# Optimization experiments

Hardware: AMD Instinct MI355X
Metric: run time of the kernel (lower is better)

The kernel has to match this reference:

```python
import jax, jax.numpy as jnp
import numpy as np

EPS_COS = 1e-8   # torch cosine_similarity eps
EPS_SHARP = 1e-6 # sharpening normalizer eps
SHIFT_RANGE = 3
MEM_WIDTH = 64


def setup_inputs() -> dict:
    key = jax.random.key(0)
    k1, k2, k3, k4, k5 = jax.random.split(key, 5)
    B, H, N, W, D = 64, 4, 16384, MEM_WIDTH, 1024
    P = W + 6  # key(W) + beta + gate + shift(3) + gamma
    return {
        "controller_state": jax.random.normal(k1, (B, D), dtype=jnp.float32),
        "prev_weights": jax.random.uniform(k2, (B, H, N), dtype=jnp.float32),
        "memory": jax.random.normal(k3, (B, N, W), dtype=jnp.float32),
        "W_read": jax.random.normal(k4, (P * H, D), dtype=jnp.float32) * 0.02,
        "b_read": jax.random.normal(k5, (P * H,), dtype=jnp.float32) * 0.02,
    }


def reference(controller_state, prev_weights, memory, W_read, b_read):
    B, H, N = prev_weights.shape
    Wd = MEM_WIDTH
    # read head parameters: [B, H, P]
    params = (controller_state @ W_read.T + b_read).reshape(B, H, -1)
    key = params[..., :Wd]                                   # [B,H,W]
    beta = jax.nn.softplus(params[..., Wd])                  # [B,H]
    gate = jax.nn.sigmoid(params[..., Wd + 1])               # [B,H]
    shift = jax.nn.softmax(params[..., Wd + 2:Wd + 2 + SHIFT_RANGE], axis=-1)  # [B,H,3]
    gamma = 1.0 + jax.nn.softplus(params[..., Wd + 2 + SHIFT_RANGE])           # [B,H]

    # content addressing: cosine similarity of key vs each memory slot
    dots = jnp.einsum('bhw,bnw->bhn', key, memory)           # [B,H,N]
    key_norm = jnp.maximum(jnp.linalg.norm(key, axis=-1), EPS_COS)        # [B,H]
    mem_norm = jnp.maximum(jnp.linalg.norm(memory, axis=-1), EPS_COS)     # [B,N]
    sim = dots / (key_norm[:, :, None] * mem_norm[:, None, :])
    content_w = jax.nn.softmax(sim * beta[:, :, None], axis=-1)           # [B,H,N]

    # interpolate with previous weights
    g = gate[:, :, None]
    gated = g * content_w + (1.0 - g) * prev_weights                     # [B,H,N]

    # circular shift: out[pos] = s0*w[pos-1] + s1*w[pos] + s2*w[pos+1]
    shifted = (shift[..., 0:1] * jnp.roll(gated, 1, axis=-1)
               + shift[..., 1:2] * gated
               + shift[..., 2:3] * jnp.roll(gated, -1, axis=-1))

    # sharpening
    sharp = shifted ** gamma[:, :, None]
    sharp = sharp / (jnp.sum(sharp, axis=-1, keepdims=True) + EPS_SHARP)
    return sharp  # [B,H,N]
```

## Files before the change

kernel.cpp:

```cpp
#include <hip/hip_runtime.h>
#include <math.h>

#define B  64
#define H  4
#define NN 16384
#define WD 64
#define DD 1024
#define PP 70

typedef float fx4 __attribute__((ext_vector_type(4)));

__device__ __forceinline__ float softplus_f(float x) {
    return fmaxf(x, 0.f) + log1pf(expf(-fabsf(x)));
}

__global__ __launch_bounds__(256) void k_params(
    const float* __restrict__ state, const float* __restrict__ Wr,
    const float* __restrict__ br, float* __restrict__ kscaled,
    float* __restrict__ coef)
{
    int bh = blockIdx.x;
    int b  = bh >> 2, h = bh & 3;
    int tid = threadIdx.x, wave = tid >> 6, lane = tid & 63;
    __shared__ float sp[PP];
    __shared__ float sbc[1];

    const float4* st4 = (const float4*)(state + (size_t)b * DD);
    for (int j = wave; j < PP; j += 4) {
        const float4* w4 = (const float4*)(Wr + (size_t)(h * PP + j) * DD);
        float acc = 0.f;
        #pragma unroll
        for (int q = 0; q < 4; ++q) {
            float4 wv = w4[lane + 64 * q];
            float4 sv = st4[lane + 64 * q];
            acc += wv.x * sv.x + wv.y * sv.y + wv.z * sv.z + wv.w * sv.w;
        }
        #pragma unroll
        for (int m = 32; m >= 1; m >>= 1) acc += __shfl_xor(acc, m, 64);
        if (lane == 0) sp[j] = acc + br[h * PP + j];
    }
    __syncthreads();
    if (tid == 0) {
        float ss = 0.f;
        for (int w = 0; w < WD; ++w) ss += sp[w] * sp[w];
        float knorm = fmaxf(sqrtf(ss), 1e-8f);
        float beta  = softplus_f(sp[64]);
        float gate  = 1.f / (1.f + expf(-sp[65]));
        float m3 = fmaxf(sp[66], fmaxf(sp[67], sp[68]));
        float e0 = expf(sp[66] - m3), e1 = expf(sp[67] - m3), e2 = expf(sp[68] - m3);
        float es = e0 + e1 + e2;
        float gamma = 1.f + softplus_f(sp[69]);
        float* c = coef + bh * 8;
        c[0] = gate; c[1] = e0 / es; c[2] = e1 / es; c[3] = e2 / es;
        c[4] = gamma; c[5] = beta;
        sbc[0] = beta / knorm;
    }
    __syncthreads();
    if (tid < WD) kscaled[bh * WD + tid] = sp[tid] * sbc[0];
}

__global__ __launch_bounds__(256) void k_sim(
    const float* __restrict__ mem, const float* __restrict__ kscaled,
    const float* __restrict__ coef, float* __restrict__ ebuf)
{
    int tid = threadIdx.x, wave = tid >> 6, lane = tid & 63;
    int blk = blockIdx.x;
    int b = blk >> 7;
    int nblk = (blk & 127) * 128;
    int r = lane >> 3, c = lane & 7;

    const float* ksb = kscaled + b * 4 * WD + c * 8;
    float4 k0a = *(const float4*)(ksb + 0 * WD);
    float4 k0b = *(const float4*)(ksb + 0 * WD + 4);
    float4 k1a = *(const float4*)(ksb + 1 * WD);
    float4 k1b = *(const float4*)(ksb + 1 * WD + 4);
    float4 k2a = *(const float4*)(ksb + 2 * WD);
    float4 k2b = *(const float4*)(ksb + 2 * WD + 4);
    float4 k3a = *(const float4*)(ksb + 3 * WD);
    float4 k3b = *(const float4*)(ksb + 3 * WD + 4);

    float bet = (c < 4) ? coef[(b * 4 + c) * 8 + 5] : 0.f;

    int nw = nblk + wave * 32;
    fx4 va[4], vb[4];
    #pragma unroll
    for (int it = 0; it < 4; ++it) {
        int n = nw + it * 8 + r;
        const fx4* rp = (const fx4*)(mem + ((size_t)b * NN + n) * WD + c * 8);
        va[it] = __builtin_nontemporal_load(rp);
        vb[it] = __builtin_nontemporal_load(rp + 1);
    }
    #pragma unroll
    for (int it = 0; it < 4; ++it) {
        fx4 v0 = va[it], v1 = vb[it];
        int n = nw + it * 8 + r;
        float d0 = v0.x*k0a.x + v0.y*k0a.y + v0.z*k0a.z + v0.w*k0a.w
                 + v1.x*k0b.x + v1.y*k0b.y + v1.z*k0b.z + v1.w*k0b.w;
        float d1 = v0.x*k1a.x + v0.y*k1a.y + v0.z*k1a.z + v0.w*k1a.w
                 + v1.x*k1b.x + v1.y*k1b.y + v1.z*k1b.z + v1.w*k1b.w;
        float d2 = v0.x*k2a.x + v0.y*k2a.y + v0.z*k2a.z + v0.w*k2a.w
                 + v1.x*k2b.x + v1.y*k2b.y + v1.z*k2b.z + v1.w*k2b.w;
        float d3 = v0.x*k3a.x + v0.y*k3a.y + v0.z*k3a.z + v0.w*k3a.w
                 + v1.x*k3b.x + v1.y*k3b.y + v1.z*k3b.z + v1.w*k3b.w;
        float q  = v0.x*v0.x + v0.y*v0.y + v0.z*v0.z + v0.w*v0.w
                 + v1.x*v1.x + v1.y*v1.y + v1.z*v1.z + v1.w*v1.w;
        #pragma unroll
        for (int m = 1; m < 8; m <<= 1) {
            d0 += __shfl_xor(d0, m, 64);
            d1 += __shfl_xor(d1, m, 64);
            d2 += __shfl_xor(d2, m, 64);
            d3 += __shfl_xor(d3, m, 64);
            q  += __shfl_xor(q,  m, 64);
        }
        if (c < 4) {
            float mn = fmaxf(sqrtf(q), 1e-8f);
            float d  = (c == 0) ? d0 : ((c == 1) ? d1 : ((c == 2) ? d2 : d3));
            ebuf[((size_t)(b * 4 + c)) * NN + n] = __expf(d / mn - bet);
        }
    }
}

__global__ __launch_bounds__(1024) void k_head(
    const float* __restrict__ ebuf, const float* __restrict__ prev,
    const float* __restrict__ coef, float* __restrict__ out)
{
    __shared__ float lds[NN];
    int bh = blockIdx.x;
    int tid = threadIdx.x, wave = tid >> 6, lane = tid & 63;
    const float* erow = ebuf + (size_t)bh * NN;
    const float* prow = prev + (size_t)bh * NN;
    float* orow = out + (size_t)bh * NN;
    const float* c = coef + bh * 8;
    float gate = c[0], sh0 = c[1], sh1 = c[2], sh2 = c[3], gamma = c[4];

    float ev[16], pw[16];
    float ls = 0.f;
    #pragma unroll
    for (int k = 0; k < 16; ++k) {
        int n = tid + k * 1024;
        ev[k] = erow[n];
        pw[k] = prow[n];
        ls += ev[k];
    }
    #pragma unroll
    for (int d = 32; d >= 1; d >>= 1) ls += __shfl_xor(ls, d, 64);
    if (lane == 0) lds[wave] = ls;
    __syncthreads();
    if (tid == 0) {
        float x = 0.f;
        for (int i = 0; i < 16; ++i) x += lds[i];
        lds[16] = x;
    }
    __syncthreads();
    float S = lds[16];
    __syncthreads();
    float ginvS = gate / S;
    float omg   = 1.f - gate;

    #pragma unroll
    for (int k = 0; k < 16; ++k) {
        int n = tid + k * 1024;
        lds[n] = ginvS * ev[k] + omg * pw[k];
    }
    __syncthreads();
    float sh[16];
    float ps = 0.f;
    #pragma unroll
    for (int k = 0; k < 16; ++k) {
        int n = tid + k * 1024;
        float gm1 = lds[(n + NN - 1) & (NN - 1)];
        float g0  = lds[n];
        float gp1 = lds[(n + 1) & (NN - 1)];
        float val = sh0 * gm1 + sh1 * g0 + sh2 * gp1;
        sh[k] = __expf(gamma * __logf(val));
        ps += sh[k];
    }
    __syncthreads();
    #pragma unroll
    for (int d = 32; d >= 1; d >>= 1) ps += __shfl_xor(ps, d, 64);
    if (lane == 0) lds[wave] = ps;
    __syncthreads();
    if (tid == 0) {
        float x = 0.f;
        for (int i = 0; i < 16; ++i) x += lds[i];
        lds[16] = x;
    }
    __syncthreads();
    float T = lds[16] + 1e-6f;
    float invT = 1.f / T;
    #pragma unroll
    for (int k = 0; k < 16; ++k) orow[tid + k * 1024] = sh[k] * invT;
}

extern "C" void kernel_launch(void* const* d_in, const int* in_sizes, int n_in,
                              void* d_out, int out_size, void* d_ws, size_t ws_size,
                              hipStream_t stream) {
    const float* state = (const float*)d_in[0];
    const float* prev  = (const float*)d_in[1];
    const float* mem   = (const float*)d_in[2];
    const float* Wr    = (const float*)d_in[3];
    const float* br    = (const float*)d_in[4];
    float* out = (float*)d_out;

    float* ebuf    = (float*)d_ws;
    float* kscaled = ebuf + (size_t)B * H * NN;
    float* coef    = kscaled + (size_t)B * H * WD;

    k_params<<<B * H, 256, 0, stream>>>(state, Wr, br, kscaled, coef);
    k_sim<<<(B * NN) / 128, 256, 0, stream>>>(mem, kscaled, coef, ebuf);
    k_head<<<B * H, 1024, 0, stream>>>(ebuf, prev, coef, out);
}
```

Measured before the change: 392.8 us.

## Vectorize head kernel with float4 chunks and LDS halo exchange

The head kernel now has each thread own contiguous float4 chunks, so loads and stores are 16-byte vector accesses. The full 64KB LDS staging of the gated row is replaced by small edge arrays that hold only each chunk's first and last element for the circular neighbour lookup. This cuts LDS traffic and lets more blocks fit per CU. The params kernel also hoists the controller-state loads out of the row loop, and prev and out use nontemporal accesses.

```diff
diff --git a/kernel.cpp b/kernel.cpp
--- a/kernel.cpp
+++ b/kernel.cpp
@@ -26,14 +26,17 @@
     __shared__ float sbc[1];
 
     const float4* st4 = (const float4*)(state + (size_t)b * DD);
+    float4 sv[4];
+    #pragma unroll
+    for (int q = 0; q < 4; ++q) sv[q] = st4[lane + 64 * q];
+
     for (int j = wave; j < PP; j += 4) {
         const float4* w4 = (const float4*)(Wr + (size_t)(h * PP + j) * DD);
         float acc = 0.f;
         #pragma unroll
         for (int q = 0; q < 4; ++q) {
             float4 wv = w4[lane + 64 * q];
-            float4 sv = st4[lane + 64 * q];
-            acc += wv.x * sv.x + wv.y * sv.y + wv.z * sv.z + wv.w * sv.w;
+            acc += wv.x * sv[q].x + wv.y * sv[q].y + wv.z * sv[q].z + wv.w * sv[q].w;
         }
         #pragma unroll
         for (int m = 32; m >= 1; m >>= 1) acc += __shfl_xor(acc, m, 64);
@@ -124,72 +127,82 @@
     const float* __restrict__ ebuf, const float* __restrict__ prev,
     const float* __restrict__ coef, float* __restrict__ out)
 {
-    __shared__ float lds[NN];
+    __shared__ float ledge[4][1024];
+    __shared__ float redge[4][1024];
+    __shared__ float redS[17];
+    __shared__ float redT[17];
     int bh = blockIdx.x;
     int tid = threadIdx.x, wave = tid >> 6, lane = tid & 63;
-    const float* erow = ebuf + (size_t)bh * NN;
-    const float* prow = prev + (size_t)bh * NN;
-    float* orow = out + (size_t)bh * NN;
+    const fx4* erow = (const fx4*)(ebuf + (size_t)bh * NN);
+    const fx4* prow = (const fx4*)(prev + (size_t)bh * NN);
+    fx4* orow = (fx4*)(out + (size_t)bh * NN);
     const float* c = coef + bh * 8;
     float gate = c[0], sh0 = c[1], sh1 = c[2], sh2 = c[3], gamma = c[4];
 
-    float ev[16], pw[16];
+    fx4 ev[4], pw[4];
     float ls = 0.f;
     #pragma unroll
-    for (int k = 0; k < 16; ++k) {
-        int n = tid + k * 1024;
-        ev[k] = erow[n];
-        pw[k] = prow[n];
-        ls += ev[k];
+    for (int k = 0; k < 4; ++k) {
+        ev[k] = erow[tid + k * 1024];
+        pw[k] = __builtin_nontemporal_load(prow + tid + k * 1024);
+        ls += ev[k].x + ev[k].y + ev[k].z + ev[k].w;
     }
     #pragma unroll
     for (int d = 32; d >= 1; d >>= 1) ls += __shfl_xor(ls, d, 64);
-    if (lane == 0) lds[wave] = ls;
+    if (lane == 0) redS[wave] = ls;
     __syncthreads();
     if (tid == 0) {
         float x = 0.f;
-        for (int i = 0; i < 16; ++i) x += lds[i];
-        lds[16] = x;
-    }
-    __syncthreads();
-    float S = lds[16];
-    __syncthreads();
+        for (int i = 0; i < 16; ++i) x += redS[i];
+        redS[16] = x;
+    }
+    __syncthreads();
+    float S = redS[16];
     float ginvS = gate / S;
     float omg   = 1.f - gate;
 
     #pragma unroll
-    for (int k = 0; k < 16; ++k) {
-        int n = tid + k * 1024;
-        lds[n] = ginvS * ev[k] + omg * pw[k];
-    }
-    __syncthreads();
-    float sh[16];
+    for (int k = 0; k < 4; ++k) {
+        ev[k] = ginvS * ev[k] + omg * pw[k];
+        ledge[k][tid] = ev[k].x;
+        redge[k][tid] = ev[k].w;
+    }
+    __syncthreads();
+
+    fx4 sh[4];
     float ps = 0.f;
     #pragma unroll
-    for (int k = 0; k < 16; ++k) {
-        int n = tid + k * 1024;
-        float gm1 = lds[(n + NN - 1) & (NN - 1)];
-        float g0  = lds[n];
-        float gp1 = lds[(n + 1) & (NN - 1)];
-        float val = sh0 * gm1 + sh1 * g0 + sh2 * gp1;
-        sh[k] = __expf(gamma * __logf(val));
-        ps += sh[k];
-    }
-    __syncthreads();
+    for (int k = 0; k < 4; ++k) {
+        float gm1 = (tid == 0)    ? redge[(k + 3) & 3][1023] : redge[k][tid - 1];
+        float gp1 = (tid == 1023) ? ledge[(k + 1) & 3][0]    : ledge[k][tid + 1];
+        fx4 g = ev[k];
+        float s0 = sh0 * gm1 + sh1 * g.x + sh2 * g.y;
+        float s1 = sh0 * g.x + sh1 * g.y + sh2 * g.z;
+        float s2 = sh0 * g.y + sh1 * g.z + sh2 * g.w;
+        float s3 = sh0 * g.z + sh1 * g.w + sh2 * gp1;
+        sh[k].x = __expf(gamma * __logf(s0));
+        sh[k].y = __expf(gamma * __logf(s1));
+        sh[k].z = __expf(gamma * __logf(s2));
+        sh[k].w = __expf(gamma * __logf(s3));
+        ps += sh[k].x + sh[k].y + sh[k].z + sh[k].w;
+    }
     #pragma unroll
     for (int d = 32; d >= 1; d >>= 1) ps += __shfl_xor(ps, d, 64);
-    if (lane == 0) lds[wave] = ps;
+    if (lane == 0) redT[wave] = ps;
     __syncthreads();
     if (tid == 0) {
         float x = 0.f;
-        for (int i = 0; i < 16; ++i) x += lds[i];
-        lds[16] = x;
-    }
-    __syncthreads();
-    float T = lds[16] + 1e-6f;
+        for (int i = 0; i < 16; ++i) x += redT[i];
+        redT[16] = x;
+    }
+    __syncthreads();
+    float T = redT[16] + 1e-6f;
     float invT = 1.f / T;
     #pragma unroll
-    for (int k = 0; k < 16; ++k) orow[tid + k * 1024] = sh[k] * invT;
+    for (int k = 0; k < 4; ++k) {
+        fx4 o = sh[k] * invT;
+        __builtin_nontemporal_store(o, orow + tid + k * 1024);
+    }
 }
 
 extern "C" void kernel_launch(void* const* d_in, const int* in_sizes, int n_in,
```

New measurement: 391.0 us. No clear change (-0.5%).
